# Performance work log

Hardware: AMD Instinct MI355X
Metric: run time of the kernel (lower is better)

## Reference

```python
import jax, jax.numpy as jnp
import numpy as np

HIDDEN = 512
NUM_HEADS = 8
HEAD = HIDDEN // NUM_HEADS
TOP_K = 64
NEG = -1e9


def setup_inputs() -> dict:
    key = jax.random.key(0)
    ks = jax.random.split(key, 12)
    B, Q, S = 2, 2048, 4096
    sc = 0.02
    return {
        "main_input": jax.random.normal(ks[0], (B, Q, HIDDEN), jnp.float32),
        "side_input": jax.random.normal(ks[1], (S, HIDDEN), jnp.float32),
        "att_mask": jax.random.randint(ks[2], (B, Q, S), 0, 2, jnp.int32),
        "Wq": jax.random.normal(ks[3], (HIDDEN, HIDDEN), jnp.float32) * sc,
        "bq": jnp.zeros((HIDDEN,), jnp.float32),
        "Wk": jax.random.normal(ks[4], (HIDDEN, HIDDEN), jnp.float32) * sc,
        "bk": jnp.zeros((HIDDEN,), jnp.float32),
        "Wv": jax.random.normal(ks[5], (HIDDEN, HIDDEN), jnp.float32) * sc,
        "bv": jnp.zeros((HIDDEN,), jnp.float32),
        "Wo": jax.random.normal(ks[6], (HIDDEN, HIDDEN), jnp.float32) * sc,
        "bo": jnp.zeros((HIDDEN,), jnp.float32),
    }


def reference(main_input, side_input, att_mask, Wq, bq, Wk, bk, Wv, bv, Wo, bo):
    B, Qlen, _ = main_input.shape
    S = side_input.shape[0]
    # multi-head projections; side K/V shared across the whole batch
    q = (main_input @ Wq + bq).reshape(B, Qlen, NUM_HEADS, HEAD)
    k = (side_input @ Wk + bk).reshape(S, NUM_HEADS, HEAD)
    v = (side_input @ Wv + bv).reshape(S, NUM_HEADS, HEAD)
    # scores: [B, H, Q, S]
    scores = jnp.einsum("bqhd,khd->bhqk", q, k) / jnp.sqrt(jnp.asarray(HEAD, q.dtype))
    # attention mask (0 = masked)
    mask = att_mask[:, None, :, :].astype(scores.dtype)  # [B,1,Q,S]
    scores = scores + (1.0 - mask) * NEG
    # top-k restriction: keep only the TOP_K largest scores per query row
    thresh = jax.lax.top_k(scores, TOP_K)[0][..., -1:]  # kth largest
    scores = jnp.where(scores >= thresh, scores, NEG)
    probs = jax.nn.softmax(scores, axis=-1)
    ctx = jnp.einsum("bhqk,khd->bqhd", probs, v).reshape(B, Qlen, HIDDEN)
    return ctx @ Wo + bo
```

## Files before the change

### kernel.cpp

```cpp
#include <hip/hip_runtime.h>
#include <stdint.h>

typedef uint32_t u32;
typedef unsigned long long u64;

#define NEGV (-1e9f)
#define NCAND 16
#define LISTCAP 256

__device__ __forceinline__ u32 f2ord(float f) {
  u32 x = __float_as_uint(f);
  return (x & 0x80000000u) ? ~x : (x | 0x80000000u);
}
__device__ __forceinline__ float ord2f(u32 u) {
  u32 x = (u & 0x80000000u) ? (u ^ 0x80000000u) : ~u;
  return __uint_as_float(x);
}

__global__ __launch_bounds__(256)
void pack_mask(const int* __restrict__ mask, u64* __restrict__ mbits) {
  int w = blockIdx.x * 256 + threadIdx.x;
  const int4* p = (const int4*)(mask + (size_t)w * 64);
  u64 bits = 0;
#pragma unroll
  for (int j = 0; j < 16; ++j) {
    int4 m = p[j];
    if (m.x) bits |= 1ull << (j * 4 + 0);
    if (m.y) bits |= 1ull << (j * 4 + 1);
    if (m.z) bits |= 1ull << (j * 4 + 2);
    if (m.w) bits |= 1ull << (j * 4 + 3);
  }
  mbits[w] = bits;
}

__global__ __launch_bounds__(256)
void gemm_bias(const float* __restrict__ A, const float* __restrict__ W,
               const float* __restrict__ bias, float* __restrict__ C) {
  __shared__ float As[16][68];
  __shared__ float Bs[16][64];
  const int tid = threadIdx.x;
  const int tx = tid & 15, ty = tid >> 4;
  const int n0 = blockIdx.x << 6, m0 = blockIdx.y << 6;
  float c[4][4] = {};
  for (int k0 = 0; k0 < 512; k0 += 16) {
    {
      const int row = tid >> 2, kp = (tid & 3) << 2;
      float4 av = *(const float4*)&A[(size_t)(m0 + row) * 512 + k0 + kp];
      As[kp + 0][row] = av.x;
      As[kp + 1][row] = av.y;
      As[kp + 2][row] = av.z;
      As[kp + 3][row] = av.w;
      const int kk = tid >> 4, np = (tid & 15) << 2;
      *(float4*)&Bs[kk][np] = *(const float4*)&W[(size_t)(k0 + kk) * 512 + n0 + np];
    }
    __syncthreads();
#pragma unroll
    for (int kk = 0; kk < 16; ++kk) {
      float4 a = *(const float4*)&As[kk][ty << 2];
      float4 b = *(const float4*)&Bs[kk][tx << 2];
      c[0][0] += a.x * b.x; c[0][1] += a.x * b.y; c[0][2] += a.x * b.z; c[0][3] += a.x * b.w;
      c[1][0] += a.y * b.x; c[1][1] += a.y * b.y; c[1][2] += a.y * b.z; c[1][3] += a.y * b.w;
      c[2][0] += a.z * b.x; c[2][1] += a.z * b.y; c[2][2] += a.z * b.z; c[2][3] += a.z * b.w;
      c[3][0] += a.w * b.x; c[3][1] += a.w * b.y; c[3][2] += a.w * b.z; c[3][3] += a.w * b.w;
    }
    __syncthreads();
  }
  float4 bv = *(const float4*)&bias[n0 + (tx << 2)];
#pragma unroll
  for (int i = 0; i < 4; ++i) {
    float4 o;
    o.x = c[i][0] + bv.x; o.y = c[i][1] + bv.y;
    o.z = c[i][2] + bv.z; o.w = c[i][3] + bv.w;
    *(float4*)&C[(size_t)(m0 + (ty << 2) + i) * 512 + n0 + (tx << 2)] = o;
  }
}

__global__ __launch_bounds__(256)
void gemm_bias_T(const float* __restrict__ A, const float* __restrict__ W,
                 const float* __restrict__ bias, float* __restrict__ CT, int qsh) {
  __shared__ float As[16][68];
  __shared__ float Bs[16][64];
  const int tid = threadIdx.x;
  const int tx = tid & 15, ty = tid >> 4;
  const int n0 = blockIdx.x << 6, m0 = blockIdx.y << 6;
  float c[4][4] = {};
  for (int k0 = 0; k0 < 512; k0 += 16) {
    {
      const int row = tid >> 2, kp = (tid & 3) << 2;
      float4 av = *(const float4*)&A[(size_t)(m0 + row) * 512 + k0 + kp];
      As[kp + 0][row] = av.x;
      As[kp + 1][row] = av.y;
      As[kp + 2][row] = av.z;
      As[kp + 3][row] = av.w;
      const int kk = tid >> 4, np = (tid & 15) << 2;
      *(float4*)&Bs[kk][np] = *(const float4*)&W[(size_t)(k0 + kk) * 512 + n0 + np];
    }
    __syncthreads();
#pragma unroll
    for (int kk = 0; kk < 16; ++kk) {
      float4 a = *(const float4*)&As[kk][ty << 2];
      float4 b = *(const float4*)&Bs[kk][tx << 2];
      c[0][0] += a.x * b.x; c[0][1] += a.x * b.y; c[0][2] += a.x * b.z; c[0][3] += a.x * b.w;
      c[1][0] += a.y * b.x; c[1][1] += a.y * b.y; c[1][2] += a.y * b.z; c[1][3] += a.y * b.w;
      c[2][0] += a.z * b.x; c[2][1] += a.z * b.y; c[2][2] += a.z * b.z; c[2][3] += a.z * b.w;
      c[3][0] += a.w * b.x; c[3][1] += a.w * b.y; c[3][2] += a.w * b.z; c[3][3] += a.w * b.w;
    }
    __syncthreads();
  }
  float4 bv = *(const float4*)&bias[n0 + (tx << 2)];
  float bvv[4] = {bv.x, bv.y, bv.z, bv.w};
  const int qlen = 1 << qsh;
  const int qmask = qlen - 1;
#pragma unroll
  for (int i = 0; i < 4; ++i) {
#pragma unroll
    for (int j = 0; j < 4; ++j) {
      float val = c[i][j] + bvv[j];
      int m = m0 + (ty << 2) + i;
      int n = n0 + (tx << 2) + j;
      int h = n >> 6, d = n & 63;
      int bb = m >> qsh, q = m & qmask;
      CT[(((size_t)bb * 8 + h) * 64 + d) * qlen + q] = val;
    }
  }
}

__global__ __launch_bounds__(256)
void score_kernel(const float* __restrict__ qT, const float* __restrict__ kT,
                  const u64* __restrict__ mbits, float* __restrict__ sbuf,
                  float* __restrict__ segmax, int sl0) {
  __shared__ float Qs[64][128];
  __shared__ float Ks[64][128];
  const int sl = sl0 + blockIdx.z;
  const int b = sl >> 3, h = sl & 7;
  const int s0 = blockIdx.x << 7, q0 = blockIdx.y << 7;
  const int tid = threadIdx.x;
  const float* qbase = qT + (size_t)sl * 64 * 2048 + q0;
  const float* kbase = kT + (size_t)h * 64 * 4096 + s0;
  float4* Qf = (float4*)&Qs[0][0];
  float4* Kf = (float4*)&Ks[0][0];
#pragma unroll
  for (int u = 0; u < 8; ++u) {
    int i = (u << 8) + tid;
    int row = i >> 5, col = (i & 31) << 2;
    Qf[i] = *(const float4*)(qbase + (size_t)row * 2048 + col);
    Kf[i] = *(const float4*)(kbase + (size_t)row * 4096 + col);
  }
  __syncthreads();
  const int tx = tid & 15, ty = tid >> 4;
  float c[8][8] = {};
#pragma unroll 4
  for (int g = 0; g < 16; ++g) {
    const int kk = g << 2;
    float qa[8][4], kb[8][4];
#pragma unroll
    for (int t = 0; t < 4; ++t) {
#pragma unroll
      for (int i = 0; i < 8; ++i) qa[i][t] = Qs[kk + t][(ty << 3) + i];
#pragma unroll
      for (int j = 0; j < 4; ++j) {
        kb[j][t]     = Ks[kk + t][(tx << 2) + j];
        kb[4 + j][t] = Ks[kk + t][64 + (tx << 2) + j];
      }
    }
#pragma unroll
    for (int i = 0; i < 8; ++i)
#pragma unroll
      for (int j = 0; j < 8; ++j)
        c[i][j] += qa[i][0] * kb[j][0] + qa[i][1] * kb[j][1]
                 + qa[i][2] * kb[j][2] + qa[i][3] * kb[j][3];
  }
  float* srow = sbuf + ((size_t)blockIdx.z * 2048 + q0) * 4096 + s0;
  const u64* mrow = mbits + ((size_t)(b * 2048 + q0)) * 64 + (s0 >> 6);
#pragma unroll
  for (int i = 0; i < 8; ++i) {
    const int row = (ty << 3) + i;
    u64 wA = mrow[(size_t)row * 64];
    u64 wB = mrow[(size_t)row * 64 + 1];
    float4 o0, o1;
    o0.x = ((wA >> ((tx << 2) + 0)) & 1) ? c[i][0] * 0.125f : NEGV;
    o0.y = ((wA >> ((tx << 2) + 1)) & 1) ? c[i][1] * 0.125f : NEGV;
    o0.z = ((wA >> ((tx << 2) + 2)) & 1) ? c[i][2] * 0.125f : NEGV;
    o0.w = ((wA >> ((tx << 2) + 3)) & 1) ? c[i][3] * 0.125f : NEGV;
    o1.x = ((wB >> ((tx << 2) + 0)) & 1) ? c[i][4] * 0.125f : NEGV;
    o1.y = ((wB >> ((tx << 2) + 1)) & 1) ? c[i][5] * 0.125f : NEGV;
    o1.z = ((wB >> ((tx << 2) + 2)) & 1) ? c[i][6] * 0.125f : NEGV;
    o1.w = ((wB >> ((tx << 2) + 3)) & 1) ? c[i][7] * 0.125f : NEGV;
    *(float4*)&srow[(size_t)row * 4096 + (tx << 2)] = o0;
    *(float4*)&srow[(size_t)row * 4096 + 64 + (tx << 2)] = o1;
    float m0 = fmaxf(fmaxf(o0.x, o0.y), fmaxf(o0.z, o0.w));
    float m1 = fmaxf(fmaxf(o1.x, o1.y), fmaxf(o1.z, o1.w));
#pragma unroll
    for (int off = 8; off; off >>= 1) {
      m0 = fmaxf(m0, __shfl_xor(m0, off, 64));
      m1 = fmaxf(m1, __shfl_xor(m1, off, 64));
    }
    if (tx == 0) {
      size_t sg = ((size_t)blockIdx.z * 2048 + q0 + row) * 64 + (s0 >> 6);
      segmax[sg] = m0;
      segmax[sg + 1] = m1;
    }
  }
}

__global__ __launch_bounds__(256)
void topk_ctx_kernel(const float* __restrict__ sbuf, const float* __restrict__ segmax,
                     const float* __restrict__ vbuf, float* __restrict__ ctxbuf,
                     int sl0) {
  const int sl = sl0 + blockIdx.y;
  const int b = sl >> 3, h = sl & 7;
  const int w = threadIdx.x >> 6, lane = threadIdx.x & 63;
  const int qi = (blockIdx.x << 2) + w;
  __shared__ u64 cand_lds[4][NCAND][64];
  u64* list = &cand_lds[w][0][0];
  const u64 lmask_lt = (1ull << lane) - 1ull;
  const u32 ordneg = f2ord(NEGV);

  const float* srow = sbuf + ((size_t)blockIdx.y * 2048 + qi) * 4096;

  float sm = segmax[((size_t)blockIdx.y * 2048 + qi) * 64 + lane];
  float fm = sm, lo0f = sm;
#pragma unroll
  for (int off = 32; off; off >>= 1) {
    fm = fmaxf(fm, __shfl_xor(fm, off, 64));
    lo0f = fminf(lo0f, __shfl_xor(lo0f, off, 64));
  }

  int cnt = 0;
#pragma unroll
  for (int jj = 0; jj < 16; jj += 4) {
    float4 v0 = *(const float4*)(srow + ((jj + 0) << 8) + (lane << 2));
    float4 v1 = *(const float4*)(srow + ((jj + 1) << 8) + (lane << 2));
    float4 v2 = *(const float4*)(srow + ((jj + 2) << 8) + (lane << 2));
    float4 v3 = *(const float4*)(srow + ((jj + 3) << 8) + (lane << 2));
    float xs[16] = {v0.x, v0.y, v0.z, v0.w, v1.x, v1.y, v1.z, v1.w,
                    v2.x, v2.y, v2.z, v2.w, v3.x, v3.y, v3.z, v3.w};
#pragma unroll
    for (int c = 0; c < 16; ++c) {
      float x = xs[c];
      if (x >= lo0f) {
        if (cnt < NCAND) {
          int sidx = ((jj + (c >> 2)) << 8) + (lane << 2) + (c & 3);
          cand_lds[w][cnt][lane] = ((u64)f2ord(x) << 32) | (u32)sidx;
        }
        cnt++;
      }
    }
  }
  const bool fb = (__ballot(cnt > NCAND) != 0ull);

  float esum = 0.f;
  int nsel = 0;
  bool meanpath = false;

  if (!fb) {
    u64 cv[NCAND];
#pragma unroll
    for (int j = 0; j < NCAND; ++j)
      cv[j] = (j < cnt) ? cand_lds[w][j][lane] : 0;
    u32 lo = f2ord(lo0f), hi = f2ord(fm) + 1;
    while (hi - lo > 1) {
      u32 mid = lo + ((hi - lo) >> 1);
      u64 mp = (u64)mid << 32;
      int c = 0;
#pragma unroll
      for (int j = 0; j < NCAND; ++j)
        c += __popcll(__ballot(cv[j] >= mp));
      if (c >= 64) lo = mid; else hi = mid;
    }
    const u64 tp = (u64)lo << 32;
    int base = 0;
#pragma unroll
    for (int j = 0; j < NCAND; ++j) {
      bool pred = cv[j] >= tp;
      u64 m = __ballot(pred);
      int ofs = base + __popcll(m & lmask_lt);
      if (pred && ofs < LISTCAP) {
        float ev = __expf(ord2f((u32)(cv[j] >> 32)) - fm);
        list[ofs] = ((u64)((u32)cv[j]) << 32) | (u64)__float_as_uint(ev);
        esum += ev;
      }
      base += (int)__popcll(m);
    }
    nsel = base < LISTCAP ? base : LISTCAP;
  } else {
    u32 lo = f2ord(lo0f), hi = f2ord(fm) + 1;
    while (hi - lo > 1) {
      u32 mid = lo + ((hi - lo) >> 1);
      float midf = ord2f(mid);
      int c = 0;
      for (int j = 0; j < 16; ++j) {
        float4 v = *(const float4*)(srow + (j << 8) + (lane << 2));
        c += __popcll(__ballot(v.x >= midf)) + __popcll(__ballot(v.y >= midf)) +
             __popcll(__ballot(v.z >= midf)) + __popcll(__ballot(v.w >= midf));
      }
      if (c >= 64) lo = mid; else hi = mid;
    }
    const float thrf = ord2f(lo);
    int base = 0;
    for (int j = 0; j < 16; ++j) {
      float4 v = *(const float4*)(srow + (j << 8) + (lane << 2));
      float xs[4] = {v.x, v.y, v.z, v.w};
#pragma unroll
      for (int cpos = 0; cpos < 4; ++cpos) {
        float x = xs[cpos];
        bool pred = (x >= thrf) && (x != NEGV);
        u64 m = __ballot(pred);
        int ofs = base + __popcll(m & lmask_lt);
        if (pred && ofs < LISTCAP) {
          int sidx = (j << 8) + (lane << 2) + cpos;
          float ev = __expf(x - fm);
          list[ofs] = ((u64)(u32)sidx << 32) | (u64)__float_as_uint(ev);
          esum += ev;
        }
        base += (int)__popcll(m);
      }
    }
    nsel = base < LISTCAP ? base : LISTCAP;
    if (base == 0) meanpath = true;
  }

#pragma unroll
  for (int off = 32; off; off >>= 1) esum += __shfl_xor(esum, off, 64);
  const float* vb = vbuf + h * 64 + lane;
  float outv;
  if (!meanpath) {
    const float rs = 1.0f / esum;
    int pad = (8 - (nsel & 7)) & 7;
    if (lane < pad && nsel + lane < LISTCAP) list[nsel + lane] = 0;
    int n8 = nsel + pad;
    if (n8 > LISTCAP) n8 = LISTCAP;
    float a0 = 0.f, a1 = 0.f, a2 = 0.f, a3 = 0.f;
    float a4 = 0.f, a5 = 0.f, a6 = 0.f, a7 = 0.f;
    for (int g = 0; g < n8; g += 8) {
      u64 p0 = list[g + 0], p1 = list[g + 1], p2 = list[g + 2], p3 = list[g + 3];
      u64 p4 = list[g + 4], p5 = list[g + 5], p6 = list[g + 6], p7 = list[g + 7];
      a0 += __uint_as_float((u32)p0) * vb[(size_t)(p0 >> 32) * 512];
      a1 += __uint_as_float((u32)p1) * vb[(size_t)(p1 >> 32) * 512];
      a2 += __uint_as_float((u32)p2) * vb[(size_t)(p2 >> 32) * 512];
      a3 += __uint_as_float((u32)p3) * vb[(size_t)(p3 >> 32) * 512];
      a4 += __uint_as_float((u32)p4) * vb[(size_t)(p4 >> 32) * 512];
      a5 += __uint_as_float((u32)p5) * vb[(size_t)(p5 >> 32) * 512];
      a6 += __uint_as_float((u32)p6) * vb[(size_t)(p6 >> 32) * 512];
      a7 += __uint_as_float((u32)p7) * vb[(size_t)(p7 >> 32) * 512];
    }
    outv = (((a0 + a1) + (a2 + a3)) + ((a4 + a5) + (a6 + a7))) * rs;
  } else {
    float acc = 0.f;
    for (int s = 0; s < 4096; ++s) acc += vb[(size_t)s * 512];
    outv = acc * (1.0f / 4096.0f);
  }
  ctxbuf[((size_t)(b * 2048 + qi)) * 512 + h * 64 + lane] = outv;
}

extern "C" void kernel_launch(void* const* d_in, const int* in_sizes, int n_in,
                              void* d_out, int out_size, void* d_ws, size_t ws_size,
                              hipStream_t stream) {
  const float* main_in = (const float*)d_in[0];
  const float* side_in = (const float*)d_in[1];
  const int*   mask    = (const int*)d_in[2];
  const float* Wq = (const float*)d_in[3];
  const float* bq = (const float*)d_in[4];
  const float* Wk = (const float*)d_in[5];
  const float* bk = (const float*)d_in[6];
  const float* Wv = (const float*)d_in[7];
  const float* bv = (const float*)d_in[8];
  const float* Wo = (const float*)d_in[9];
  const float* bo = (const float*)d_in[10];
  float* out = (float*)d_out;

  char* ws = (char*)d_ws;
  float* qT   = (float*)(ws);
  float* kT   = (float*)(ws + ((size_t)8 << 20));
  float* vbuf = (float*)(ws + ((size_t)16 << 20));
  float* ctxb = (float*)(ws + ((size_t)24 << 20));
  u64* mbits  = (u64*)(ws + ((size_t)32 << 20));
  const size_t base = (size_t)34 << 20;
  const size_t sliceb = (size_t)2048 * 4096 * 4;
  const size_t segb   = (size_t)2048 * 64 * 4;
  const size_t per = sliceb + segb;

  int nz = 1;
  if (ws_size > base + per) {
    size_t m = (ws_size - base) / per;
    nz = (int)(m > 16 ? 16 : m);
  }
  float* sbuf = (float*)(ws + base);
  float* smax = (float*)(ws + base + (size_t)nz * sliceb);

  pack_mask<<<1024, 256, 0, stream>>>(mask, mbits);
  gemm_bias_T<<<dim3(8, 64), 256, 0, stream>>>(main_in, Wq, bq, qT, 11);
  gemm_bias_T<<<dim3(8, 64), 256, 0, stream>>>(side_in, Wk, bk, kT, 12);
  gemm_bias  <<<dim3(8, 64), 256, 0, stream>>>(side_in, Wv, bv, vbuf);

  for (int sl0 = 0; sl0 < 16; sl0 += nz) {
    int z = nz < (16 - sl0) ? nz : (16 - sl0);
    score_kernel   <<<dim3(32, 16, z), 256, 0, stream>>>(qT, kT, mbits, sbuf, smax, sl0);
    topk_ctx_kernel<<<dim3(512, z), 256, 0, stream>>>(sbuf, smax, vbuf, ctxb, sl0);
  }

  gemm_bias<<<dim3(8, 64), 256, 0, stream>>>(ctxb, Wo, bo, out);
}
```

Baseline: 819.6 us.

## Refine segment maxima to 32-wide and skip loading low-max segments in top-k

The score kernel now writes per-row maxima over 32-column segments (128 per row) instead of 64-column segments. The top-k kernel finds the 64th-largest segment max as a tighter lower bound and reads only the segments whose max reaches it, each lane scanning contiguous 32-element chunks. This avoids reading the whole 4096-wide score row per query. The score kernel also stages Q/K in two 32-row halves to halve shared memory, and the slice batch count is capped at 4, which adds launches but gives a smaller cache footprint.

New measurement: 754.1 us. -8.0%, faster.

```diff
diff --git a/kernel.cpp b/kernel.cpp
--- a/kernel.cpp
+++ b/kernel.cpp
@@ -129,46 +129,49 @@
 void score_kernel(const float* __restrict__ qT, const float* __restrict__ kT,
                   const u64* __restrict__ mbits, float* __restrict__ sbuf,
                   float* __restrict__ segmax, int sl0) {
-  __shared__ float Qs[64][128];
-  __shared__ float Ks[64][128];
+  __shared__ float Qs[32][128];
+  __shared__ float Ks[32][128];
   const int sl = sl0 + blockIdx.z;
   const int b = sl >> 3, h = sl & 7;
   const int s0 = blockIdx.x << 7, q0 = blockIdx.y << 7;
   const int tid = threadIdx.x;
   const float* qbase = qT + (size_t)sl * 64 * 2048 + q0;
   const float* kbase = kT + (size_t)h * 64 * 4096 + s0;
+  const int tx = tid & 15, ty = tid >> 4;
   float4* Qf = (float4*)&Qs[0][0];
   float4* Kf = (float4*)&Ks[0][0];
-#pragma unroll
-  for (int u = 0; u < 8; ++u) {
-    int i = (u << 8) + tid;
-    int row = i >> 5, col = (i & 31) << 2;
-    Qf[i] = *(const float4*)(qbase + (size_t)row * 2048 + col);
-    Kf[i] = *(const float4*)(kbase + (size_t)row * 4096 + col);
-  }
-  __syncthreads();
-  const int tx = tid & 15, ty = tid >> 4;
   float c[8][8] = {};
+  for (int half = 0; half < 2; ++half) {
+#pragma unroll
+    for (int u = 0; u < 4; ++u) {
+      int i = (u << 8) + tid;
+      int row = i >> 5, col = (i & 31) << 2;
+      Qf[i] = *(const float4*)(qbase + (size_t)(half * 32 + row) * 2048 + col);
+      Kf[i] = *(const float4*)(kbase + (size_t)(half * 32 + row) * 4096 + col);
+    }
+    __syncthreads();
 #pragma unroll 4
-  for (int g = 0; g < 16; ++g) {
-    const int kk = g << 2;
-    float qa[8][4], kb[8][4];
-#pragma unroll
-    for (int t = 0; t < 4; ++t) {
-#pragma unroll
-      for (int i = 0; i < 8; ++i) qa[i][t] = Qs[kk + t][(ty << 3) + i];
-#pragma unroll
-      for (int j = 0; j < 4; ++j) {
-        kb[j][t]     = Ks[kk + t][(tx << 2) + j];
-        kb[4 + j][t] = Ks[kk + t][64 + (tx << 2) + j];
+    for (int g = 0; g < 8; ++g) {
+      const int kk = g << 2;
+      float qa[8][4], kb[8][4];
+#pragma unroll
+      for (int t = 0; t < 4; ++t) {
+#pragma unroll
+        for (int i = 0; i < 8; ++i) qa[i][t] = Qs[kk + t][(ty << 3) + i];
+#pragma unroll
+        for (int j = 0; j < 4; ++j) {
+          kb[j][t]     = Ks[kk + t][(tx << 2) + j];
+          kb[4 + j][t] = Ks[kk + t][64 + (tx << 2) + j];
+        }
       }
-    }
-#pragma unroll
-    for (int i = 0; i < 8; ++i)
-#pragma unroll
-      for (int j = 0; j < 8; ++j)
-        c[i][j] += qa[i][0] * kb[j][0] + qa[i][1] * kb[j][1]
-                 + qa[i][2] * kb[j][2] + qa[i][3] * kb[j][3];
+#pragma unroll
+      for (int i = 0; i < 8; ++i)
+#pragma unroll
+        for (int j = 0; j < 8; ++j)
+          c[i][j] += qa[i][0] * kb[j][0] + qa[i][1] * kb[j][1]
+                   + qa[i][2] * kb[j][2] + qa[i][3] * kb[j][3];
+    }
+    __syncthreads();
   }
   float* srow = sbuf + ((size_t)blockIdx.z * 2048 + q0) * 4096 + s0;
   const u64* mrow = mbits + ((size_t)(b * 2048 + q0)) * 64 + (s0 >> 6);
@@ -191,14 +194,14 @@
     float m0 = fmaxf(fmaxf(o0.x, o0.y), fmaxf(o0.z, o0.w));
     float m1 = fmaxf(fmaxf(o1.x, o1.y), fmaxf(o1.z, o1.w));
 #pragma unroll
-    for (int off = 8; off; off >>= 1) {
+    for (int off = 4; off; off >>= 1) {
       m0 = fmaxf(m0, __shfl_xor(m0, off, 64));
       m1 = fmaxf(m1, __shfl_xor(m1, off, 64));
     }
-    if (tx == 0) {
-      size_t sg = ((size_t)blockIdx.z * 2048 + q0 + row) * 64 + (s0 >> 6);
+    if ((tx & 7) == 0) {
+      size_t sg = ((size_t)blockIdx.z * 2048 + q0 + row) * 128 + (s0 >> 5) + (tx >> 3);
       segmax[sg] = m0;
-      segmax[sg + 1] = m1;
+      segmax[sg + 2] = m1;
     }
   }
 }
@@ -218,32 +221,58 @@
 
   const float* srow = sbuf + ((size_t)blockIdx.y * 2048 + qi) * 4096;
 
-  float sm = segmax[((size_t)blockIdx.y * 2048 + qi) * 64 + lane];
-  float fm = sm, lo0f = sm;
+  float2 smv = *(const float2*)(segmax + ((size_t)blockIdx.y * 2048 + qi) * 128 + (lane << 1));
+  u32 so0 = f2ord(smv.x), so1 = f2ord(smv.y);
+  u32 mxo = so0 > so1 ? so0 : so1;
+  u32 mno = so0 < so1 ? so0 : so1;
 #pragma unroll
   for (int off = 32; off; off >>= 1) {
-    fm = fmaxf(fm, __shfl_xor(fm, off, 64));
-    lo0f = fminf(lo0f, __shfl_xor(lo0f, off, 64));
-  }
+    u32 a = (u32)__shfl_xor((int)mxo, off, 64);
+    u32 c = (u32)__shfl_xor((int)mno, off, 64);
+    mxo = a > mxo ? a : mxo;
+    mno = c < mno ? c : mno;
+  }
+  const float fm = ord2f(mxo);
+  {
+    u32 lo = mno, hi = mxo + 1;
+    while (hi - lo > 1) {
+      u32 mid = lo + ((hi - lo) >> 1);
+      int c = __popcll(__ballot(so0 >= mid)) + __popcll(__ballot(so1 >= mid));
+      if (c >= 64) lo = mid; else hi = mid;
+    }
+    mno = lo;
+  }
+  const u32 ordT = mno;
+  const float Tf = ord2f(ordT);
 
   int cnt = 0;
-#pragma unroll
-  for (int jj = 0; jj < 16; jj += 4) {
-    float4 v0 = *(const float4*)(srow + ((jj + 0) << 8) + (lane << 2));
-    float4 v1 = *(const float4*)(srow + ((jj + 1) << 8) + (lane << 2));
-    float4 v2 = *(const float4*)(srow + ((jj + 2) << 8) + (lane << 2));
-    float4 v3 = *(const float4*)(srow + ((jj + 3) << 8) + (lane << 2));
-    float xs[16] = {v0.x, v0.y, v0.z, v0.w, v1.x, v1.y, v1.z, v1.w,
-                    v2.x, v2.y, v2.z, v2.w, v3.x, v3.y, v3.z, v3.w};
-#pragma unroll
-    for (int c = 0; c < 16; ++c) {
-      float x = xs[c];
-      if (x >= lo0f) {
-        if (cnt < NCAND) {
-          int sidx = ((jj + (c >> 2)) << 8) + (lane << 2) + (c & 3);
-          cand_lds[w][cnt][lane] = ((u64)f2ord(x) << 32) | (u32)sidx;
+  const float* lbase = srow + (lane << 6);
+#pragma unroll
+  for (int reg = 0; reg < 2; ++reg) {
+    bool active = (reg == 0) ? (smv.x >= Tf) : (smv.y >= Tf);
+    if (active) {
+      const float* rb = lbase + (reg << 5);
+      float4 v0 = *(const float4*)(rb + 0);
+      float4 v1 = *(const float4*)(rb + 4);
+      float4 v2 = *(const float4*)(rb + 8);
+      float4 v3 = *(const float4*)(rb + 12);
+      float4 v4 = *(const float4*)(rb + 16);
+      float4 v5 = *(const float4*)(rb + 20);
+      float4 v6 = *(const float4*)(rb + 24);
+      float4 v7 = *(const float4*)(rb + 28);
+      float xs[32] = {v0.x, v0.y, v0.z, v0.w, v1.x, v1.y, v1.z, v1.w,
+                      v2.x, v2.y, v2.z, v2.w, v3.x, v3.y, v3.z, v3.w,
+                      v4.x, v4.y, v4.z, v4.w, v5.x, v5.y, v5.z, v5.w,
+                      v6.x, v6.y, v6.z, v6.w, v7.x, v7.y, v7.z, v7.w};
+#pragma unroll
+      for (int cc = 0; cc < 32; ++cc) {
+        if (xs[cc] >= Tf) {
+          if (cnt < NCAND) {
+            int sidx = (lane << 6) + (reg << 5) + cc;
+            cand_lds[w][cnt][lane] = ((u64)f2ord(xs[cc]) << 32) | (u32)sidx;
+          }
+          cnt++;
         }
-        cnt++;
       }
     }
   }
@@ -258,7 +287,7 @@
 #pragma unroll
     for (int j = 0; j < NCAND; ++j)
       cv[j] = (j < cnt) ? cand_lds[w][j][lane] : 0;
-    u32 lo = f2ord(lo0f), hi = f2ord(fm) + 1;
+    u32 lo = ordT, hi = mxo + 1;
     while (hi - lo > 1) {
       u32 mid = lo + ((hi - lo) >> 1);
       u64 mp = (u64)mid << 32;
@@ -284,7 +313,7 @@
     }
     nsel = base < LISTCAP ? base : LISTCAP;
   } else {
-    u32 lo = f2ord(lo0f), hi = f2ord(fm) + 1;
+    u32 lo = ordT, hi = mxo + 1;
     while (hi - lo > 1) {
       u32 mid = lo + ((hi - lo) >> 1);
       float midf = ord2f(mid);
@@ -377,13 +406,13 @@
   u64* mbits  = (u64*)(ws + ((size_t)32 << 20));
   const size_t base = (size_t)34 << 20;
   const size_t sliceb = (size_t)2048 * 4096 * 4;
-  const size_t segb   = (size_t)2048 * 64 * 4;
+  const size_t segb   = (size_t)2048 * 128 * 4;
   const size_t per = sliceb + segb;
 
   int nz = 1;
   if (ws_size > base + per) {
     size_t m = (ws_size - base) / per;
-    nz = (int)(m > 16 ? 16 : m);
+    nz = (int)(m > 4 ? 4 : m);
   }
   float* sbuf = (float*)(ws + base);
   float* smax = (float*)(ws + base + (size_t)nz * sliceb);
```
